# Kernel tuning notes

Measured on AMD Instinct MI355X. Metric: run time of the kernel, lower is better.

The kernel has to match this reference:

```python
import jax, jax.numpy as jnp
import numpy as np

B, S, D = 4, 128, 4096
H, KV, HD = 32, 8, 128
REP = H // KV  # GQA repeat factor = 4


def setup_inputs() -> dict:
    key = jax.random.key(0)
    ks = jax.random.split(key, 10)
    scale = 0.02
    x = jax.random.normal(ks[0], (B, S, D), dtype=jnp.float32)
    # projection weights stored as (in, out) so y = x @ W + b (== torch Linear)
    wq = jax.random.normal(ks[1], (D, H * HD), dtype=jnp.float32) * scale
    bq = jax.random.normal(ks[2], (H * HD,), dtype=jnp.float32) * scale
    wk = jax.random.normal(ks[3], (D, KV * HD), dtype=jnp.float32) * scale
    bk = jax.random.normal(ks[4], (KV * HD,), dtype=jnp.float32) * scale
    wv = jax.random.normal(ks[5], (D, KV * HD), dtype=jnp.float32) * scale
    bv = jax.random.normal(ks[6], (KV * HD,), dtype=jnp.float32) * scale
    wo = jax.random.normal(ks[7], (H * HD, D), dtype=jnp.float32) * scale
    bo = jax.random.normal(ks[8], (D,), dtype=jnp.float32) * scale
    # rotary frequencies: theta=10000, half-dim = HD//2 = 64
    inv_freq = 1.0 / (10000.0 ** (jnp.arange(0, HD, 2, dtype=jnp.float32) / HD))
    t = jnp.arange(S, dtype=jnp.float32)
    angles = jnp.outer(t, inv_freq)  # (S, 64)
    freqs_cos = jnp.cos(angles)
    freqs_sin = jnp.sin(angles)
    # additive causal mask (S, S): 0 on/below diagonal, -inf above
    mask = jnp.where(jnp.tril(jnp.ones((S, S), dtype=bool)), 0.0, -jnp.inf).astype(jnp.float32)
    cache_k = jnp.zeros((B, S, KV, HD), dtype=jnp.float32)
    cache_v = jnp.zeros((B, S, KV, HD), dtype=jnp.float32)
    return {
        "x": x, "start_pos": 0, "freqs_cos": freqs_cos, "freqs_sin": freqs_sin,
        "mask": mask, "cache_k": cache_k, "cache_v": cache_v,
        "wq": wq, "bq": bq, "wk": wk, "bk": bk, "wv": wv, "bv": bv,
        "wo": wo, "bo": bo,
    }


def _rope(t, cos, sin):
    # t: (B, S, h, HD); treat last dim as HD//2 complex pairs (real, imag)
    tr = t.reshape(*t.shape[:-1], HD // 2, 2)
    tre, tim = tr[..., 0], tr[..., 1]
    c = cos[None, :, None, :]  # (1, S, 1, HD//2)
    s = sin[None, :, None, :]
    out_re = tre * c - tim * s
    out_im = tre * s + tim * c
    return jnp.stack([out_re, out_im], axis=-1).reshape(t.shape)


def reference(x, start_pos, freqs_cos, freqs_sin, mask, cache_k, cache_v,
              wq, bq, wk, bk, wv, bv, wo, bo):
    bsz, seq_len, _ = x.shape
    q = (x @ wq + bq).reshape(bsz, seq_len, H, HD)
    k = (x @ wk + bk).reshape(bsz, seq_len, KV, HD)
    v = (x @ wv + bv).reshape(bsz, seq_len, KV, HD)
    q = _rope(q, freqs_cos, freqs_sin)
    k = _rope(k, freqs_cos, freqs_sin)
    # KV-cache append (functional)
    cache_k = cache_k.at[:bsz, start_pos:start_pos + seq_len].set(k)
    cache_v = cache_v.at[:bsz, start_pos:start_pos + seq_len].set(v)
    keys = cache_k[:bsz, :start_pos + seq_len]    # (B, T, KV, HD)
    vals = cache_v[:bsz, :start_pos + seq_len]
    # GQA head expansion (repeat_interleave on head dim)
    keys = jnp.repeat(keys, REP, axis=2)          # (B, T, H, HD)
    vals = jnp.repeat(vals, REP, axis=2)
    scale = 1.0 / jnp.sqrt(jnp.float32(HD))
    scores = jnp.einsum('bqhd,bkhd->bhqk', q, keys) * scale + mask
    attn = jax.nn.softmax(scores, axis=-1)
    out = jnp.einsum('bhqk,bkhd->bqhd', attn, vals).reshape(bsz, seq_len, H * HD)
    return out @ wo + bo
```

## Files before the change

### kernel.cpp

```cpp
#include <hip/hip_runtime.h>
#include <math.h>


#define B_   4
#define S_   128
#define D_   4096
#define H_   32
#define KV_  8
#define HD_  128
#define M_   (B_ * S_)
#define NQKV 6144
#define SCALE_ 0.088388347648318447f

typedef _Float16 half_t;
typedef half_t f16x8 __attribute__((ext_vector_type(8)));
typedef float  f32x4 __attribute__((ext_vector_type(4)));

__device__ inline void load_lds16(const void* g, void* l) {
    __builtin_amdgcn_global_load_lds((const __attribute__((address_space(1))) void*)g,
                                     (__attribute__((address_space(3))) void*)l,
                                     16, 0, 0);
}

__device__ void transpose_tile(const float* __restrict__ src, int Nsrc, int nsrc0,
                               int ndst0, int k0, int Ntot,
                               half_t* __restrict__ Wt, void* ldsraw) {
    float (*tile)[132] = (float(*)[132])ldsraw;
    const int t = threadIdx.x;
#pragma unroll
    for (int p = 0; p < 8; ++p) {
        int idx = t + p * 256;
        int r = idx >> 5, c4 = idx & 31;
        *(float4*)&tile[r][c4 * 4] =
            *(const float4*)&src[(size_t)(k0 + r) * Nsrc + nsrc0 + c4 * 4];
    }
    __syncthreads();
    const int n = t >> 1, kh = t & 1;
    __align__(16) half_t hs[32];
#pragma unroll
    for (int i = 0; i < 32; ++i)
        hs[i] = (half_t)tile[kh * 32 + i][n];
    size_t ob = ((size_t)(k0 >> 6) * Ntot + ndst0 + n) * 64 + kh * 32;
#pragma unroll
    for (int u = 0; u < 4; ++u)
        *(uint4*)&Wt[ob + u * 8] = *(uint4*)&hs[u * 8];
}

__global__ __launch_bounds__(256)
void prep_qkv(const float* __restrict__ wq, const float* __restrict__ wk,
              const float* __restrict__ wv, const float* __restrict__ x,
              half_t* __restrict__ Wt, half_t* __restrict__ x16) {
    __shared__ __align__(16) char lds[33792];
    const int bx = blockIdx.x;
    if (bx < 3072) {
        int nt = bx % 48, kt = bx / 48;
        const float* src; int Nsrc, ns0, nd0;
        if (nt < 32)      { src = wq; Nsrc = 4096; ns0 = nt * 128;        nd0 = nt * 128; }
        else if (nt < 40) { src = wk; Nsrc = 1024; ns0 = (nt - 32) * 128; nd0 = 4096 + (nt - 32) * 128; }
        else              { src = wv; Nsrc = 1024; ns0 = (nt - 40) * 128; nd0 = 5120 + (nt - 40) * 128; }
        transpose_tile(src, Nsrc, ns0, nd0, kt * 64, NQKV, Wt, lds);
    } else {
        int i0 = (bx - 3072) * 1024 + threadIdx.x;
#pragma unroll
        for (int j = 0; j < 4; ++j) {
            int i = i0 + j * 256;
            float4 f = ((const float4*)x)[i];
            __align__(8) half_t h4[4] = {(half_t)f.x, (half_t)f.y, (half_t)f.z, (half_t)f.w};
            ((uint2*)x16)[i] = *(uint2*)h4;
        }
    }
}

__device__ __forceinline__ void stage64x128(const half_t* __restrict__ A,
                                            const half_t* __restrict__ Bbase,
                                            int N, int m0, int n0, int kc,
                                            half_t* AsD, half_t* BsD, int tid) {
    const int lane = tid & 63, tB = tid & 192;
    const half_t* Bslab = Bbase + ((size_t)(kc >> 6) * N + n0) * 64;
#pragma unroll
    for (int p = 0; p < 2; ++p) {
        int tb = p * 256 + tB;
        int task = tb + lane;
        int r = task >> 3, os = (task ^ r) & 7;
        load_lds16(&A[(size_t)(m0 + r) * 4096 + kc + os * 8], AsD + tb * 8);
    }
#pragma unroll
    for (int p = 0; p < 4; ++p) {
        int tb = p * 256 + tB;
        int task = tb + lane;
        int r = task >> 3, os = (task ^ r) & 7;
        load_lds16(&Bslab[(size_t)r * 64 + os * 8], BsD + tb * 8);
    }
}

__device__ __forceinline__ void compute64x128(const half_t* AsD, const half_t* BsD,
                                              int tid, f32x4 (&acc)[4][2]) {
    const int lane = tid & 63;
    const int quad = lane >> 4, l16 = lane & 15;
    const int wn = (tid >> 6) * 32;
    half_t (*As)[64] = (half_t(*)[64])AsD;
    half_t (*Bs)[64] = (half_t(*)[64])BsD;
#pragma unroll
    for (int kk = 0; kk < 2; ++kk) {
        f16x8 af[4], bf[2];
        int L = kk * 4 + quad;
#pragma unroll
        for (int i = 0; i < 4; ++i) {
            int ra = i * 16 + l16;
            af[i] = *(const f16x8*)&As[ra][(L ^ (ra & 7)) * 8];
        }
#pragma unroll
        for (int j = 0; j < 2; ++j) {
            int rb = wn + j * 16 + l16;
            bf[j] = *(const f16x8*)&Bs[rb][(L ^ (rb & 7)) * 8];
        }
#pragma unroll
        for (int i = 0; i < 4; ++i)
#pragma unroll
            for (int j = 0; j < 2; ++j)
                acc[i][j] = __builtin_amdgcn_mfma_f32_16x16x32_f16(af[i], bf[j], acc[i][j], 0, 0, 0);
    }
}

__device__ __forceinline__ void fence_step(int n) {
    if (n == 6)      asm volatile("s_waitcnt vmcnt(6)" ::: "memory");
    else if (n == 0) asm volatile("s_waitcnt vmcnt(0)" ::: "memory");
    __builtin_amdgcn_s_barrier();
    __builtin_amdgcn_sched_barrier(0);
}

__device__ __forceinline__ void gemm64x128(const half_t* __restrict__ A,
                                           const half_t* __restrict__ Bbase,
                                           int N, int m0, int n0, char* lds,
                                           f32x4 (&acc)[4][2]) {
    const int tid = threadIdx.x;
    half_t* As0 = (half_t*)lds;
    half_t* Bs0 = (half_t*)(lds + 24576);
    stage64x128(A, Bbase, N, m0, n0, 0,  As0,        Bs0,        tid);
    stage64x128(A, Bbase, N, m0, n0, 64, As0 + 4096, Bs0 + 8192, tid);
    fence_step(6);
    int cur = 0, pf = 2;
    for (int it = 0; it < 62; ++it) {
        stage64x128(A, Bbase, N, m0, n0, (it + 2) * 64,
                    As0 + pf * 4096, Bs0 + pf * 8192, tid);
        compute64x128(As0 + cur * 4096, Bs0 + cur * 8192, tid, acc);
        fence_step(6);
        cur = (cur == 2) ? 0 : cur + 1;
        pf  = (pf  == 2) ? 0 : pf  + 1;
    }
    compute64x128(As0 + cur * 4096, Bs0 + cur * 8192, tid, acc);
    fence_step(0);
    cur = (cur == 2) ? 0 : cur + 1;
    compute64x128(As0 + cur * 4096, Bs0 + cur * 8192, tid, acc);
    __syncthreads();
}

__global__ __launch_bounds__(256, 2)
void gemm_qkv_fused(const half_t* __restrict__ x16, const half_t* __restrict__ Wt,
                    const float* __restrict__ bq, const float* __restrict__ bk,
                    const float* __restrict__ bv, const float* __restrict__ fc,
                    const float* __restrict__ fs, half_t* __restrict__ q16,
                    half_t* __restrict__ k16, half_t* __restrict__ vt16) {
    __shared__ __align__(16) char lds[73728];
    const int bx = blockIdx.x;
    const int o = (bx & 7) * 48 + (bx >> 3);
    const int nb = o >> 3, mb = o & 7;
    const int m0 = mb * 64, n0 = nb * 128;

    f32x4 acc[4][2] = {};
    gemm64x128(x16, Wt, NQKV, m0, n0, lds, acc);

    const int tid = threadIdx.x;
    const int lane = tid & 63;
    const int quad = lane >> 4, l16 = lane & 15;
    const int wn = (tid >> 6) * 32;

    if (n0 < 5120) {
        const bool isQ = n0 < 4096;
        const float* bias = isQ ? bq : bk;
        const int bOff = isQ ? 0 : 4096;
        half_t* dst = isQ ? q16 : k16;
        const int ldd = isQ ? 4096 : 1024;
#pragma unroll
        for (int i = 0; i < 4; ++i)
#pragma unroll
            for (int j = 0; j < 2; ++j) {
                const int col = n0 + wn + j * 16 + l16;
                const int d2 = (col >> 1) & 63;
                const float bcol = bias[col - bOff];
#pragma unroll
                for (int rg = 0; rg < 4; ++rg) {
                    const int row = m0 + i * 16 + quad * 4 + rg;
                    float v = acc[i][j][rg] + bcol;
                    float p = __shfl_xor(v, 1);
                    const int iloc = row & 127;
                    const float c = fc[iloc * 64 + d2], sn = fs[iloc * 64 + d2];
                    float ov = (l16 & 1) ? (p * sn + v * c)
                                         : (v * c - p * sn);
                    float o2 = __shfl_xor(ov, 1);
                    if (!(l16 & 1)) {
                        __align__(4) half_t hh[2] = {(half_t)ov, (half_t)o2};
                        *(unsigned int*)&dst[(size_t)row * ldd + (col - bOff)] =
                            *(unsigned int*)hh;
                    }
                }
            }
    } else {
        half_t (*Th)[136] = (half_t(*)[136])lds;
#pragma unroll
        for (int i = 0; i < 4; ++i)
#pragma unroll
            for (int j = 0; j < 2; ++j) {
                const int cl = wn + j * 16 + l16;
                const float bcol = bv[n0 - 5120 + cl];
#pragma unroll
                for (int rg = 0; rg < 4; ++rg)
                    Th[i * 16 + quad * 4 + rg][cl] = (half_t)(acc[i][j][rg] + bcol);
            }
        __syncthreads();
        const int d = tid >> 1, ih = tid & 1;
        const int kv = (n0 - 5120) >> 7;
        const int b = mb >> 1, i0 = (mb & 1) * 64;
        __align__(16) half_t hs[32];
#pragma unroll
        for (int u = 0; u < 32; ++u) hs[u] = Th[ih * 32 + u][d];
        size_t base = ((size_t)(b * 8 + kv) * 128 + d) * 128 + i0 + ih * 32;
#pragma unroll
        for (int u = 0; u < 4; ++u)
            *(uint4*)&vt16[base + u * 8] = *(uint4*)&hs[u * 8];
    }
}

__global__ __launch_bounds__(256, 2)
void attn_wo(const half_t* __restrict__ q16, const half_t* __restrict__ k16,
             const half_t* __restrict__ vt16, half_t* __restrict__ a16,
             const float* __restrict__ wo, half_t* __restrict__ WtO) {
    __shared__ __align__(16) char lds[62464];
    if (blockIdx.x >= 512) {
        int t = blockIdx.x - 512;
        transpose_tile(wo, 4096, (t & 31) * 128, (t & 31) * 128, (t >> 5) * 64,
                       4096, WtO, lds);
        return;
    }
    half_t (*Qs)[136] = (half_t(*)[136])lds;
    half_t (*Ks)[136] = (half_t(*)[136])(lds + 8704);
    float (*Ps)[132]  = (float(*)[132])(lds + 43520);
    float (*red)[16]  = (float(*)[16])(lds + 60416);

    const int tid = threadIdx.x;
    const int qi = blockIdx.x & 3, h = (blockIdx.x >> 2) & 31, b = blockIdx.x >> 7;
    const int kv = h >> 2;
    const int qbase = qi * 32;
    const int lane = tid & 63, w = tid >> 6;
    const int quad = lane >> 4, l16 = lane & 15;
    const int m0 = (w & 1) * 16, half64 = (w >> 1) * 64;

#pragma unroll
    for (int p = 0; p < 2; ++p) {
        int task = tid + p * 256;
        int r = task >> 4, c = task & 15;
        *(uint4*)&Qs[r][c * 8] =
            *(const uint4*)&q16[((size_t)(b * 128 + qbase + r) * 32 + h) * 128 + c * 8];
    }
#pragma unroll
    for (int p = 0; p < 8; ++p) {
        int task = tid + p * 256;
        int r = task >> 4, c = task & 15;
        *(uint4*)&Ks[r][c * 8] =
            *(const uint4*)&k16[((size_t)(b * 128 + r) * 8 + kv) * 128 + c * 8];
    }
    __syncthreads();

    f32x4 s[4] = {};
#pragma unroll
    for (int kc = 0; kc < 4; ++kc) {
        f16x8 af = *(const f16x8*)&Qs[m0 + l16][kc * 32 + quad * 8];
#pragma unroll
        for (int jb = 0; jb < 4; ++jb) {
            f16x8 bf = *(const f16x8*)&Ks[half64 + jb * 16 + l16][kc * 32 + quad * 8];
            s[jb] = __builtin_amdgcn_mfma_f32_16x16x32_f16(af, bf, s[jb], 0, 0, 0);
        }
    }
#pragma unroll
    for (int jb = 0; jb < 4; ++jb) {
        int j = half64 + jb * 16 + l16;
#pragma unroll
        for (int rg = 0; rg < 4; ++rg) {
            int row = m0 + quad * 4 + rg;
            Ps[row][j] = (j <= qbase + row) ? s[jb][rg] * SCALE_ : -1e30f;
        }
    }
    __syncthreads();

    const int r = tid >> 3, seg = tid & 7;
    float mx = -1e30f;
#pragma unroll
    for (int i = 0; i < 16; ++i) mx = fmaxf(mx, Ps[r][seg * 16 + i]);
    red[r][seg] = mx;
    __syncthreads();

    uint4 vstage[8];
#pragma unroll
    for (int p = 0; p < 8; ++p) {
        int task = tid + p * 256;
        int rr = task >> 4, c = task & 15;
        vstage[p] = *(const uint4*)&vt16[((size_t)(b * 8 + kv) * 128 + rr) * 128 + c * 8];
    }
    float m = red[r][0];
#pragma unroll
    for (int i = 1; i < 8; ++i) m = fmaxf(m, red[r][i]);
    float sum = 0.f;
#pragma unroll
    for (int i = 0; i < 16; ++i) {
        float e = __expf(Ps[r][seg * 16 + i] - m);
        Ps[r][seg * 16 + i] = e;
        sum += e;
    }
    red[r][8 + seg] = sum;
#pragma unroll
    for (int p = 0; p < 8; ++p) {
        int task = tid + p * 256;
        int rr = task >> 4, c = task & 15;
        *(uint4*)&Ks[rr][c * 8] = vstage[p];
    }
    __syncthreads();

    float tot = 0.f;
#pragma unroll
    for (int i = 0; i < 8; ++i) tot += red[r][8 + i];
    float inv = 1.0f / tot;
#pragma unroll
    for (int i = 0; i < 16; ++i)
        Qs[r][seg * 16 + i] = (half_t)(Ps[r][seg * 16 + i] * inv);
    __syncthreads();

    f32x4 o[4] = {};
#pragma unroll
    for (int jc = 0; jc < 4; ++jc) {
        f16x8 af = *(const f16x8*)&Qs[m0 + l16][jc * 32 + quad * 8];
#pragma unroll
        for (int db = 0; db < 4; ++db) {
            f16x8 bf = *(const f16x8*)&Ks[half64 + db * 16 + l16][jc * 32 + quad * 8];
            o[db] = __builtin_amdgcn_mfma_f32_16x16x32_f16(af, bf, o[db], 0, 0, 0);
        }
    }
#pragma unroll
    for (int db = 0; db < 4; ++db) {
        int d = half64 + db * 16 + l16;
#pragma unroll
        for (int rg = 0; rg < 4; ++rg) {
            int row = m0 + quad * 4 + rg;
            a16[(size_t)(b * 128 + qbase + row) * 4096 + h * 128 + d] = (half_t)o[db][rg];
        }
    }
}

__global__ __launch_bounds__(256, 2)
void gemm_o_fused(const half_t* __restrict__ a16, const half_t* __restrict__ WtO,
                  const float* __restrict__ bo, float* __restrict__ out) {
    __shared__ __align__(16) char lds[73728];
    const int bx = blockIdx.x;
    const int o = (bx & 7) * 32 + (bx >> 3);
    const int nb = o >> 3, mb = o & 7;
    const int m0 = mb * 64, n0 = nb * 128;

    f32x4 acc[4][2] = {};
    gemm64x128(a16, WtO, 4096, m0, n0, lds, acc);

    const int tid = threadIdx.x;
    const int lane = tid & 63;
    const int quad = lane >> 4, l16 = lane & 15;
    const int wn = (tid >> 6) * 32;
#pragma unroll
    for (int i = 0; i < 4; ++i)
#pragma unroll
        for (int j = 0; j < 2; ++j) {
            const int col = n0 + wn + j * 16 + l16;
            const float bcol = bo[col];
#pragma unroll
            for (int rg = 0; rg < 4; ++rg) {
                const int row = m0 + i * 16 + quad * 4 + rg;
                out[(size_t)row * 4096 + col] = acc[i][j][rg] + bcol;
            }
        }
}

extern "C" void kernel_launch(void* const* d_in, const int* in_sizes, int n_in,
                              void* d_out, int out_size, void* d_ws, size_t ws_size,
                              hipStream_t stream) {
    const float* x    = (const float*)d_in[0];
    const float* fc   = (const float*)d_in[2];
    const float* fs   = (const float*)d_in[3];
    const float* wq   = (const float*)d_in[7];
    const float* bq   = (const float*)d_in[8];
    const float* wk   = (const float*)d_in[9];
    const float* bk   = (const float*)d_in[10];
    const float* wv   = (const float*)d_in[11];
    const float* bv   = (const float*)d_in[12];
    const float* wo   = (const float*)d_in[13];
    const float* bo   = (const float*)d_in[14];
    float* out = (float*)d_out;

    half_t* x16  = (half_t*)d_ws;
    half_t* a16  = x16 + 2097152;
    half_t* q16  = a16 + 2097152;
    half_t* k16  = q16 + 2097152;
    half_t* vt16 = k16 + 524288;
    half_t* Wt   = vt16 + 524288;
    half_t* WtO  = Wt;

    prep_qkv<<<3584, 256, 0, stream>>>(wq, wk, wv, x, Wt, x16);

    gemm_qkv_fused<<<384, 256, 0, stream>>>(x16, Wt, bq, bk, bv, fc, fs,
                                            q16, k16, vt16);

    attn_wo<<<2560, 256, 0, stream>>>(q16, k16, vt16, a16, wo, WtO);

    gemm_o_fused<<<256, 256, 0, stream>>>(a16, WtO, bo, out);
}
```

Before: 283.1 us.

## Move Wo transpose into QKV GEMM launch and raise MFMA wave priority

The fp32-to-fp16 transpose of wo now runs as 2048 extra blocks inside the QKV GEMM launch instead of inside the attention launch. This lets that memory-bound conversion overlap with the compute-bound GEMM, which has only 384 tiles, and leaves attention as a lean 512-block kernel. WtO gets its own workspace region instead of aliasing Wt, since Wt is still being read while WtO is written. The QKV GEMM also wraps its MFMA bursts in s_setprio(1), so its waves are scheduled ahead of the co-resident transpose blocks. Risk: the transpose blocks may compete for memory bandwidth with the GEMM loads, and the workspace footprint grows.

```diff
diff --git a/kernel.cpp b/kernel.cpp
--- a/kernel.cpp
+++ b/kernel.cpp
@@ -93,6 +93,7 @@
     }
 }
 
+template <bool PRIO>
 __device__ __forceinline__ void compute64x128(const half_t* AsD, const half_t* BsD,
                                               int tid, f32x4 (&acc)[4][2]) {
     const int lane = tid & 63;
@@ -114,11 +115,13 @@
             int rb = wn + j * 16 + l16;
             bf[j] = *(const f16x8*)&Bs[rb][(L ^ (rb & 7)) * 8];
         }
+        if (PRIO) __builtin_amdgcn_s_setprio(1);
 #pragma unroll
         for (int i = 0; i < 4; ++i)
 #pragma unroll
             for (int j = 0; j < 2; ++j)
                 acc[i][j] = __builtin_amdgcn_mfma_f32_16x16x32_f16(af[i], bf[j], acc[i][j], 0, 0, 0);
+        if (PRIO) __builtin_amdgcn_s_setprio(0);
     }
 }
 
@@ -129,6 +132,7 @@
     __builtin_amdgcn_sched_barrier(0);
 }
 
+template <bool PRIO>
 __device__ __forceinline__ void gemm64x128(const half_t* __restrict__ A,
                                            const half_t* __restrict__ Bbase,
                                            int N, int m0, int n0, char* lds,
@@ -143,32 +147,39 @@
     for (int it = 0; it < 62; ++it) {
         stage64x128(A, Bbase, N, m0, n0, (it + 2) * 64,
                     As0 + pf * 4096, Bs0 + pf * 8192, tid);
-        compute64x128(As0 + cur * 4096, Bs0 + cur * 8192, tid, acc);
+        compute64x128<PRIO>(As0 + cur * 4096, Bs0 + cur * 8192, tid, acc);
         fence_step(6);
         cur = (cur == 2) ? 0 : cur + 1;
         pf  = (pf  == 2) ? 0 : pf  + 1;
     }
-    compute64x128(As0 + cur * 4096, Bs0 + cur * 8192, tid, acc);
+    compute64x128<PRIO>(As0 + cur * 4096, Bs0 + cur * 8192, tid, acc);
     fence_step(0);
     cur = (cur == 2) ? 0 : cur + 1;
-    compute64x128(As0 + cur * 4096, Bs0 + cur * 8192, tid, acc);
+    compute64x128<PRIO>(As0 + cur * 4096, Bs0 + cur * 8192, tid, acc);
     __syncthreads();
 }
 
 __global__ __launch_bounds__(256, 2)
-void gemm_qkv_fused(const half_t* __restrict__ x16, const half_t* __restrict__ Wt,
-                    const float* __restrict__ bq, const float* __restrict__ bk,
-                    const float* __restrict__ bv, const float* __restrict__ fc,
-                    const float* __restrict__ fs, half_t* __restrict__ q16,
-                    half_t* __restrict__ k16, half_t* __restrict__ vt16) {
+void gemm_qkv_pack(const half_t* __restrict__ x16, const half_t* __restrict__ Wt,
+                   const float* __restrict__ bq, const float* __restrict__ bk,
+                   const float* __restrict__ bv, const float* __restrict__ fc,
+                   const float* __restrict__ fs, half_t* __restrict__ q16,
+                   half_t* __restrict__ k16, half_t* __restrict__ vt16,
+                   const float* __restrict__ wo, half_t* __restrict__ WtO) {
     __shared__ __align__(16) char lds[73728];
     const int bx = blockIdx.x;
+    if (bx >= 384) {
+        int t = bx - 384;
+        transpose_tile(wo, 4096, (t & 31) * 128, (t & 31) * 128, (t >> 5) * 64,
+                       4096, WtO, lds);
+        return;
+    }
     const int o = (bx & 7) * 48 + (bx >> 3);
     const int nb = o >> 3, mb = o & 7;
     const int m0 = mb * 64, n0 = nb * 128;
 
     f32x4 acc[4][2] = {};
-    gemm64x128(x16, Wt, NQKV, m0, n0, lds, acc);
+    gemm64x128<true>(x16, Wt, NQKV, m0, n0, lds, acc);
 
     const int tid = threadIdx.x;
     const int lane = tid & 63;
@@ -232,16 +243,9 @@
 }
 
 __global__ __launch_bounds__(256, 2)
-void attn_wo(const half_t* __restrict__ q16, const half_t* __restrict__ k16,
-             const half_t* __restrict__ vt16, half_t* __restrict__ a16,
-             const float* __restrict__ wo, half_t* __restrict__ WtO) {
+void fused_attn(const half_t* __restrict__ q16, const half_t* __restrict__ k16,
+                const half_t* __restrict__ vt16, half_t* __restrict__ a16) {
     __shared__ __align__(16) char lds[62464];
-    if (blockIdx.x >= 512) {
-        int t = blockIdx.x - 512;
-        transpose_tile(wo, 4096, (t & 31) * 128, (t & 31) * 128, (t >> 5) * 64,
-                       4096, WtO, lds);
-        return;
-    }
     half_t (*Qs)[136] = (half_t(*)[136])lds;
     half_t (*Ks)[136] = (half_t(*)[136])(lds + 8704);
     float (*Ps)[132]  = (float(*)[132])(lds + 43520);
@@ -365,7 +369,7 @@
     const int m0 = mb * 64, n0 = nb * 128;
 
     f32x4 acc[4][2] = {};
-    gemm64x128(a16, WtO, 4096, m0, n0, lds, acc);
+    gemm64x128<false>(a16, WtO, 4096, m0, n0, lds, acc);
 
     const int tid = threadIdx.x;
     const int lane = tid & 63;
@@ -407,14 +411,14 @@
     half_t* k16  = q16 + 2097152;
     half_t* vt16 = k16 + 524288;
     half_t* Wt   = vt16 + 524288;
-    half_t* WtO  = Wt;
+    half_t* WtO  = Wt + 25165824;
 
     prep_qkv<<<3584, 256, 0, stream>>>(wq, wk, wv, x, Wt, x16);
 
-    gemm_qkv_fused<<<384, 256, 0, stream>>>(x16, Wt, bq, bk, bv, fc, fs,
-                                            q16, k16, vt16);
-
-    attn_wo<<<2560, 256, 0, stream>>>(q16, k16, vt16, a16, wo, WtO);
+    gemm_qkv_pack<<<384 + 2048, 256, 0, stream>>>(x16, Wt, bq, bk, bv, fc, fs,
+                                                  q16, k16, vt16, wo, WtO);
+
+    fused_attn<<<512, 256, 0, stream>>>(q16, k16, vt16, a16);
 
     gemm_o_fused<<<256, 256, 0, stream>>>(a16, WtO, bo, out);
 }
```

Result: no change. 282.0 us (-0.4%).
